# Kernel optimization log

Measured on AMD Instinct MI355X. Metric: run time of the kernel, lower is better.

## Reference

```python
import jax, jax.numpy as jnp
import numpy as np

HID = 64
INIT_N = 1000   # init_target_num
OUT_N = 50      # out_tar_num
XL = 64         # x_len
PI = float(np.pi)
SMALL = 1e-6
TEMP = 0.01


def _ln(x, g, b):
    m = jnp.mean(x, axis=-1, keepdims=True)
    v = jnp.mean((x - m) ** 2, axis=-1, keepdims=True)
    return (x - m) * jax.lax.rsqrt(v + 1e-5) * g + b


def _smooth_l1(p, t):
    d = jnp.abs(p - t)
    return jnp.mean(jnp.where(d < 1.0, 0.5 * d * d, d - 0.5))


def setup_inputs() -> dict:
    key = jax.random.key(0)
    ks = jax.random.split(key, 24)
    B, M = 512, 2000
    D = XL * 2 + 2  # 130
    f32 = jnp.float32

    def lin(k, i, o):
        return (jax.random.normal(k, (i, o), f32) / np.sqrt(i)).astype(f32)

    return {
        'osm': jax.random.normal(ks[0], (B, M, 4), f32),
        'agent_traj': jax.random.normal(ks[1], (B, XL), f32),
        'vectornet_feature': jax.random.normal(ks[2], (B, XL), f32),
        'end': jax.random.normal(ks[3], (B, 2), f32),
        'speed': jax.random.normal(ks[4], (B, 2), f32),
        # offsetx_pre: Linear(D,64) -> LN -> GELU -> Linear(64,2)
        'ox_w1': lin(ks[5], D, HID), 'ox_b1': jnp.zeros((HID,), f32),
        'ox_g1': jnp.ones((HID,), f32), 'ox_be1': jnp.zeros((HID,), f32),
        'ox_w2': lin(ks[6], HID, 2), 'ox_b2': jnp.zeros((2,), f32),
        # target_proj: Linear(D,64)->LN->GELU->Linear(64,64)->LN->GELU->Linear(64,2)
        'tp_w1': lin(ks[7], D, HID), 'tp_b1': jnp.zeros((HID,), f32),
        'tp_g1': jnp.ones((HID,), f32), 'tp_be1': jnp.zeros((HID,), f32),
        'tp_w2': lin(ks[8], HID, HID), 'tp_b2': jnp.zeros((HID,), f32),
        'tp_g2': jnp.ones((HID,), f32), 'tp_be2': jnp.zeros((HID,), f32),
        'tp_w3': lin(ks[9], HID, 2), 'tp_b3': jnp.zeros((2,), f32),
    }


def reference(osm, agent_traj, vectornet_feature, end, speed,
              ox_w1, ox_b1, ox_g1, ox_be1, ox_w2, ox_b2,
              tp_w1, tp_b1, tp_g1, tp_be1, tp_w2, tp_b2, tp_g2, tp_be2, tp_w3, tp_b3):
    B = osm.shape[0]
    # --- select INIT_N closest osm points (else-branch of original) ---
    osm_points = osm[:, :, :2]                                # [B,M,2]
    dist = jnp.sqrt(jnp.sum(osm_points ** 2, axis=2))         # [B,M]
    idx = jnp.argsort(dist, axis=1)[:, :INIT_N]               # [B,N]
    pts = jnp.take_along_axis(osm_points, idx[..., None], axis=1)  # [B,N,2]

    at = jnp.broadcast_to(agent_traj[:, None, :], (B, INIT_N, XL))
    vf = jnp.broadcast_to(vectornet_feature[:, None, :], (B, INIT_N, XL))

    # --- offsetx_pre MLP ---
    feat = jnp.concatenate([vf, at, pts], axis=-1)            # [B,N,130]
    h = jax.nn.gelu(_ln(feat @ ox_w1 + ox_b1, ox_g1, ox_be1), approximate=False)
    offset_x = h @ ox_w2 + ox_b2                              # [B,N,2]
    targets = pts + offset_x

    # --- target_proj MLP ---
    feat2 = jnp.concatenate([vf, at, targets], axis=-1)
    h = jax.nn.gelu(_ln(feat2 @ tp_w1 + tp_b1, tp_g1, tp_be1), approximate=False)
    h = jax.nn.gelu(_ln(h @ tp_w2 + tp_b2, tp_g2, tp_be2), approximate=False)
    targets = h @ tp_w3 + tp_b3                               # [B,N,2]

    # --- gaussian-like policy score over candidates ---
    mean = jnp.mean(targets, axis=1, keepdims=True)           # [B,1,2]
    var = jnp.var(targets, axis=1, keepdims=True, ddof=1)     # unbiased, like torch.var
    pdx = jnp.exp(-0.5 * (targets[..., 0] - mean[..., 0]) ** 2 / var[..., 0] + SMALL) \
          / jnp.sqrt(2.0 * PI * var[..., 0] + SMALL)
    pdy = jnp.exp(-0.5 * (targets[..., 1] - mean[..., 1]) ** 2 / var[..., 1] + SMALL) \
          / jnp.sqrt(2.0 * PI * var[..., 1] + SMALL)
    policy_dist = pdx * pdy                                   # [B,N]

    end_b = end[:, None, :]                                   # [B,1,2]
    L_off = _smooth_l1(targets, end_b)

    d = jnp.sqrt(jnp.sum((pts - end_b) ** 2, axis=2))         # [B,N]
    soft = jax.nn.softmax(-d / TEMP, axis=1)
    target_index = jnp.argmax(soft, axis=1)                   # [B]

    # CrossEntropyLoss(policy_dist as logits, target_index), mean reduction
    lse = jax.nn.logsumexp(policy_dist, axis=1)               # [B]
    picked = jnp.take_along_axis(policy_dist, target_index[:, None], axis=1)[:, 0]
    L_cls = jnp.mean(lse - picked)

    # top-k targets by policy_dist (descending)
    p_index = jnp.argsort(-policy_dist, axis=1)[:, :OUT_N]    # [B,K]
    top_targets = jnp.take_along_axis(targets, p_index[..., None], axis=1)  # [B,K,2]
    L_end = _smooth_l1(top_targets, end_b)

    return (L_cls, L_off + L_end * 3.0, top_targets)
```

## Files before the change

kernel.cpp:

```cpp
#include <hip/hip_runtime.h>
#include <math.h>

#define NT 256
#define NB 512
#define NP 2000
#define NS 1000
#define NO 50

typedef unsigned int u32;
typedef unsigned long long u64;
typedef unsigned short u16;
typedef unsigned char u8;
typedef __attribute__((ext_vector_type(8))) short short8;
typedef __attribute__((ext_vector_type(4))) float f32x4;

__device__ __forceinline__ float sl1(float x){ float d = fabsf(x); return d < 1.f ? 0.5f*d*d : d - 0.5f; }

__device__ __forceinline__ u32 mono(float f){
  u32 u = __float_as_uint(f);
  return u ^ ((u >> 31) ? 0xFFFFFFFFu : 0x80000000u);
}
__device__ __forceinline__ float dist_rn(float x, float y){
  return __fsqrt_rn(__fadd_rn(__fmul_rn(x,x), __fmul_rn(y,y)));
}
__device__ __forceinline__ float rl(float v, int l){
  return __builtin_bit_cast(float, __builtin_amdgcn_readlane(__builtin_bit_cast(int, v), l));
}
__device__ __forceinline__ u16 f2bf(float f){
  u32 u = __float_as_uint(f);
  u32 r = (u + 0x7FFFu + ((u >> 16) & 1u)) >> 16;
  return (u16)r;
}
__device__ __forceinline__ float bf2f(u16 h){ return __uint_as_float(((u32)h) << 16); }

__device__ __forceinline__ float gelu_(float x){
  float z = x * 0.70710678118654752440f;
  float az = fabsf(z);
  float t = __frcp_rn(fmaf(0.3275911f, az, 1.0f));
  float p =          fmaf(t, 1.061405429f, -1.453152027f);
  p = fmaf(p, t, 1.421413741f);
  p = fmaf(p, t, -0.284496736f);
  p = fmaf(p, t, 0.254829592f);
  p = p * t;
  float e = __expf(-az*az);
  float er = fmaf(-p, e, 1.0f);
  er = copysignf(er, z);
  float hx = 0.5f * x;
  return fmaf(hx, er, hx);
}
__device__ __forceinline__ float wred(float v){
  #pragma unroll
  for (int s = 1; s < 64; s <<= 1) v += __shfl_xor(v, s, 64);
  return v;
}
__device__ __forceinline__ float bsum(float v, float* s, int tid){
  #pragma unroll
  for (int o = 32; o > 0; o >>= 1) v += __shfl_down(v, o, 64);
  __syncthreads();
  if ((tid & 63) == 0) s[tid >> 6] = v;
  __syncthreads();
  return (s[0]+s[1])+(s[2]+s[3]);
}
__device__ __forceinline__ float bmax(float v, float* s, int tid){
  #pragma unroll
  for (int o = 32; o > 0; o >>= 1) v = fmaxf(v, __shfl_down(v, o, 64));
  __syncthreads();
  if ((tid & 63) == 0) s[tid >> 6] = v;
  __syncthreads();
  return fmaxf(fmaxf(s[0],s[1]), fmaxf(s[2],s[3]));
}
__device__ __forceinline__ u32 bminu32(u32 v, u32* s, int tid){
  #pragma unroll
  for (int o = 32; o > 0; o >>= 1){ u32 w = __shfl_down(v, o, 64); v = w < v ? w : v; }
  __syncthreads();
  if ((tid & 63) == 0) s[tid >> 6] = v;
  __syncthreads();
  u32 a = s[0] < s[1] ? s[0] : s[1];
  u32 c = s[2] < s[3] ? s[2] : s[3];
  return a < c ? a : c;
}
__device__ __forceinline__ u64 bminu64(u64 v, u64* s, int tid){
  #pragma unroll
  for (int o = 32; o > 0; o >>= 1){ u64 w = __shfl_down(v, o, 64); v = w < v ? w : v; }
  __syncthreads();
  if ((tid & 63) == 0) s[tid >> 6] = v;
  __syncthreads();
  u64 a = s[0] < s[1] ? s[0] : s[1];
  u64 c = s[2] < s[3] ? s[2] : s[3];
  return a < c ? a : c;
}

__global__ void init_k(double* acc){
  if (threadIdx.x < 8) acc[threadIdx.x] = 0.0;
}

__global__ __launch_bounds__(NT) void main_k(
    const float* __restrict__ osm, const float* __restrict__ agent, const float* __restrict__ vect,
    const float* __restrict__ endp,
    const float* __restrict__ oxw1, const float* __restrict__ oxb1, const float* __restrict__ oxg1, const float* __restrict__ oxbe1,
    const float* __restrict__ oxw2, const float* __restrict__ oxb2,
    const float* __restrict__ tpw1, const float* __restrict__ tpb1, const float* __restrict__ tpg1, const float* __restrict__ tpbe1,
    const float* __restrict__ tpw2, const float* __restrict__ tpb2, const float* __restrict__ tpg2, const float* __restrict__ tpbe2,
    const float* __restrict__ tpw3, const float* __restrict__ tpb3,
    float* __restrict__ out, double* __restrict__ acc)
{
  const int b = blockIdx.x;
  const int tid = threadIdx.x;
  const int lane = tid & 63;
  const int wv = tid >> 6;
  const int lm = lane & 15;
  const int q  = lane >> 4;

  __shared__ u32 keys32[2048];
  __shared__ u8  state[2048];
  __shared__ u32 hist[256];
  __shared__ u32 wtot[4];
  __shared__ u32 sc[8];
  __shared__ u16 sIdx[1024];
  __shared__ float2 ptf2[NS];
  __shared__ float2 tg[NS];
  __shared__ float pol[NS];
  __shared__ float vfs[64], ats[64];
  __shared__ float foxA[64], foxB[64], foxC[64];
  __shared__ float ftpA[64], ftpB[64], ftpC[64];
  __shared__ float w2aS[64], w2bS[64];
  __shared__ float scox[6], sctp[6];
  __shared__ float redf[4];
  __shared__ u32 redu[4];
  __shared__ u64 redk[4];
  __shared__ u16 list50[64];
  __shared__ __align__(16) u16 trans[4][2][16][72];

  const float2* osm2 = (const float2*)osm;
  const float ex = endp[b*2 + 0], ey = endp[b*2 + 1];

  if (tid < 64){ vfs[tid] = vect[b*64 + tid]; ats[tid] = agent[b*64 + tid]; }
  for (int i = tid; i < NP; i += NT){
    float2 P = osm2[((size_t)b*NP + i)*2];
    keys32[i] = mono(dist_rn(P.x, P.y));
  }
  for (int i = tid; i < 2048; i += NT) state[i] = (i < NP) ? (u8)2 : (u8)0;
  if (tid == 0){ sc[0] = NS; sc[2] = 0; }
  __syncthreads();

  {
    float* part = (float*)&trans[0][0][0][0];
    int ch = tid & 63, grp = tid >> 6;
    float pox = 0.f, ptp = 0.f;
    for (int k = grp*32; k < grp*32 + 32; ++k){
      float f = (k < 64) ? vfs[k] : ats[k-64];
      pox = fmaf(f, oxw1[k*64 + ch], pox);
      ptp = fmaf(f, tpw1[k*64 + ch], ptp);
    }
    part[grp*64 + ch] = pox;
    part[(grp+4)*64 + ch] = ptp;
    __syncthreads();
    if (tid < 64){
      float bo = oxb1[tid] + ((part[0*64+tid]+part[1*64+tid])+(part[2*64+tid]+part[3*64+tid]));
      float bt = tpb1[tid] + ((part[4*64+tid]+part[5*64+tid])+(part[6*64+tid]+part[7*64+tid]));
      float cxo = oxw1[128*64 + tid], cyo = oxw1[129*64 + tid];
      float cxt = tpw1[128*64 + tid], cyt = tpw1[129*64 + tid];
      const float inv64 = 1.0f/64.0f;
      float mb = wred(bo)*inv64, mx_ = wred(cxo)*inv64, my_ = wred(cyo)*inv64;
      float e0 = bo - mb, e1 = cxo - mx_, e2 = cyo - my_;
      float g = oxg1[tid];
      foxA[tid] = e0*g; foxB[tid] = e1*g; foxC[tid] = e2*g;
      float E00 = wred(e0*e0)*inv64, E11 = wred(e1*e1)*inv64, E22 = wred(e2*e2)*inv64;
      float E01 = wred(e0*e1)*inv64, E02 = wred(e0*e2)*inv64, E12 = wred(e1*e2)*inv64;
      if (tid == 0){ scox[0]=E00; scox[1]=E11; scox[2]=E22; scox[3]=E01; scox[4]=E02; scox[5]=E12; }
      float mb2 = wred(bt)*inv64, mx2 = wred(cxt)*inv64, my2 = wred(cyt)*inv64;
      float f0 = bt - mb2, f1 = cxt - mx2, f2 = cyt - my2;
      float gt_ = tpg1[tid];
      ftpA[tid] = f0*gt_; ftpB[tid] = f1*gt_; ftpC[tid] = f2*gt_;
      float F00 = wred(f0*f0)*inv64, F11 = wred(f1*f1)*inv64, F22 = wred(f2*f2)*inv64;
      float F01 = wred(f0*f1)*inv64, F02 = wred(f0*f2)*inv64, F12 = wred(f1*f2)*inv64;
      if (tid == 0){ sctp[0]=F00; sctp[1]=F11; sctp[2]=F22; sctp[3]=F01; sctp[4]=F02; sctp[5]=F12; }
      w2aS[tid] = oxw2[2*tid]; w2bS[tid] = oxw2[2*tid + 1];
    }
  }
  __syncthreads();

  {
    const int plist[6] = {7,6,5,4,1,0};
    for (int pi = 0; pi < 6; ++pi){
      if (sc[2]) break;
      const int p = plist[pi];
      hist[tid] = 0; __syncthreads();
      for (int i = tid; i < NP; i += NT) if (state[i] == 2){
        int bb = (p >= 4) ? (int)((keys32[i] >> ((p-4)*8)) & 255) : (int)((((u32)i) >> (p*8)) & 255);
        atomicAdd(&hist[bb], 1u);
      }
      __syncthreads();
      u32 myc = hist[tid], v = myc;
      { int l_ = tid & 63;
        #pragma unroll
        for (int s = 1; s < 64; s <<= 1){ u32 n = __shfl_up(v, s, 64); if (l_ >= s) v += n; }
        if (l_ == 63) wtot[tid >> 6] = v;
      }
      __syncthreads();
      u32 add = 0;
      #pragma unroll
      for (int w = 0; w < 4; ++w) if (w < (tid >> 6)) add += wtot[w];
      u32 myinc = v + add;
      u32 Krem = sc[0];
      bool iamp = false; u32 exc = myinc - myc;
      if (myc > 0 && exc <= Krem-1 && Krem-1 < myinc){ sc[1] = (u32)tid; iamp = true; }
      __syncthreads();
      u32 pb = sc[1];
      for (int i = tid; i < NP; i += NT) if (state[i] == 2){
        int bb = (p >= 4) ? (int)((keys32[i] >> ((p-4)*8)) & 255) : (int)((((u32)i) >> (p*8)) & 255);
        state[i] = (bb < (int)pb) ? (u8)1 : (bb > (int)pb) ? (u8)0 : (u8)2;
      }
      if (iamp){ u32 nk = Krem - exc; sc[0] = nk; if (nk == myc) sc[2] = 1; }
      __syncthreads();
    }
    if (tid == 0) sc[4] = 0;
    __syncthreads();
    for (int i = tid; i < NP; i += NT) if (state[i] != 0){
      u32 pos = atomicAdd(&sc[4], 1u);
      sIdx[pos] = (u16)i;
      ptf2[pos] = osm2[((size_t)b*NP + i)*2];
    }
    __syncthreads();
  }

  const float foxAv = foxA[lane], foxBv = foxB[lane], foxCv = foxC[lane], beoxv = oxbe1[lane];
  const float ftpAv = ftpA[lane], ftpBv = ftpB[lane], ftpCv = ftpC[lane], be2v = tpbe1[lane];
  const float so0 = scox[0], so1 = scox[1], so2 = scox[2], so3 = scox[3], so4 = scox[4], so5 = scox[5];
  const float st0 = sctp[0], st1 = sctp[1], st2 = sctp[2], st3 = sctp[3], st4 = sctp[4], st5 = sctp[5];
  const float oxb20 = oxb2[0], oxb21 = oxb2[1], tpb30 = tpb3[0], tpb31 = tpb3[1];
  float g3c[4], be3c[4], b2i[4], w3a[4], w3b[4];
  #pragma unroll
  for (int nt = 0; nt < 4; ++nt){
    int ch = lm + 16*nt;
    g3c[nt] = tpg2[ch]; be3c[nt] = tpbe2[ch]; b2i[nt] = tpb2[ch];
    w3a[nt] = tpw3[ch*2]; w3b[nt] = tpw3[ch*2 + 1];
  }
  short8 bh[2][4], bl[2][4];
  #pragma unroll
  for (int kt = 0; kt < 2; ++kt)
    #pragma unroll
    for (int nt = 0; nt < 4; ++nt){
      short8 H, L;
      #pragma unroll
      for (int j = 0; j < 8; ++j){
        float w = tpw2[(kt*32 + q*8 + j)*64 + nt*16 + lm];
        u16 hh = f2bf(w);
        H[j] = (short)hh;
        L[j] = (short)f2bf(w - bf2f(hh));
      }
      bh[kt][nt] = H; bl[kt][nt] = L;
    }

  u16* trh  = &trans[wv][0][0][0];
  u16* trl_ = &trans[wv][1][0][0];
  float* trf = (float*)&trans[wv][0][0][0];
  float loff = 0.f;

  for (int t = wv; t < 63; t += 4){
    const int pbase = t*16;
    int sp = pbase + lm; if (sp > NS-1) sp = NS-1;
    const float2 P = ptf2[sp];
    const float px = P.x, py = P.y;
    float var1 = so0 + px*px*so1 + py*py*so2 + 2.0f*(px*so3 + py*so4 + px*py*so5);
    const float r1 = __frsqrt_rn(var1 + 1e-5f);
    #pragma unroll
    for (int p = 0; p < 16; ++p){
      float spx = rl(px,p), spy = rl(py,p), sr = rl(r1,p);
      float vv = fmaf(sr, fmaf(spy, foxCv, fmaf(spx, foxBv, foxAv)), beoxv);
      trf[p*68 + lane] = gelu_(vv);
    }
    f32x4 ga = *(f32x4*)&trf[lm*68 + q*16 + 0];
    f32x4 gb = *(f32x4*)&trf[lm*68 + q*16 + 4];
    f32x4 gc = *(f32x4*)&trf[lm*68 + q*16 + 8];
    f32x4 gd = *(f32x4*)&trf[lm*68 + q*16 + 12];
    f32x4 wa0 = *(f32x4*)&w2aS[q*16+0], wa1 = *(f32x4*)&w2aS[q*16+4], wa2 = *(f32x4*)&w2aS[q*16+8], wa3 = *(f32x4*)&w2aS[q*16+12];
    f32x4 wb0 = *(f32x4*)&w2bS[q*16+0], wb1 = *(f32x4*)&w2bS[q*16+4], wb2 = *(f32x4*)&w2bS[q*16+8], wb3 = *(f32x4*)&w2bS[q*16+12];
    float o0 = 0.f, o1 = 0.f;
    #pragma unroll
    for (int j = 0; j < 4; ++j){
      o0 = fmaf(ga[j],wa0[j], fmaf(gb[j],wa1[j], fmaf(gc[j],wa2[j], fmaf(gd[j],wa3[j], o0))));
      o1 = fmaf(ga[j],wb0[j], fmaf(gb[j],wb1[j], fmaf(gc[j],wb2[j], fmaf(gd[j],wb3[j], o1))));
    }
    o0 += __shfl_xor(o0,16,64); o0 += __shfl_xor(o0,32,64);
    o1 += __shfl_xor(o1,16,64); o1 += __shfl_xor(o1,32,64);
    const float tx = px + o0 + oxb20;
    const float ty = py + o1 + oxb21;
    float var2 = st0 + tx*tx*st1 + ty*ty*st2 + 2.0f*(tx*st3 + ty*st4 + tx*ty*st5);
    const float r2 = __frsqrt_rn(var2 + 1e-5f);
    #pragma unroll
    for (int p = 0; p < 16; ++p){
      float stx = rl(tx,p), sty = rl(ty,p), sr = rl(r2,p);
      float vv = fmaf(sr, fmaf(sty, ftpCv, fmaf(stx, ftpBv, ftpAv)), be2v);
      vv = gelu_(vv);
      u16 hh = f2bf(vv);
      trh[p*72 + lane]  = hh;
      trl_[p*72 + lane] = f2bf(vv - bf2f(hh));
    }
    short8 ah0 = *(short8*)&trh[lm*72 + q*8];
    short8 ah1 = *(short8*)&trh[lm*72 + 32 + q*8];
    short8 al0 = *(short8*)&trl_[lm*72 + q*8];
    short8 al1 = *(short8*)&trl_[lm*72 + 32 + q*8];
    f32x4 accv[4];
    #pragma unroll
    for (int nt = 0; nt < 4; ++nt){
      f32x4 c; c[0] = c[1] = c[2] = c[3] = b2i[nt];
      c = __builtin_amdgcn_mfma_f32_16x16x32_bf16(ah0, bh[0][nt], c, 0,0,0);
      c = __builtin_amdgcn_mfma_f32_16x16x32_bf16(ah1, bh[1][nt], c, 0,0,0);
      c = __builtin_amdgcn_mfma_f32_16x16x32_bf16(ah0, bl[0][nt], c, 0,0,0);
      c = __builtin_amdgcn_mfma_f32_16x16x32_bf16(ah1, bl[1][nt], c, 0,0,0);
      c = __builtin_amdgcn_mfma_f32_16x16x32_bf16(al0, bh[0][nt], c, 0,0,0);
      c = __builtin_amdgcn_mfma_f32_16x16x32_bf16(al1, bh[1][nt], c, 0,0,0);
      accv[nt] = c;
    }
    float sP[4], qP[4];
    #pragma unroll
    for (int e = 0; e < 4; ++e){
      float a0 = accv[0][e], a1 = accv[1][e], a2 = accv[2][e], a3 = accv[3][e];
      sP[e] = (a0+a1)+(a2+a3);
      qP[e] = fmaf(a0,a0, fmaf(a1,a1, fmaf(a2,a2, a3*a3)));
    }
    #pragma unroll
    for (int s_ = 1; s_ < 16; s_ <<= 1){
      #pragma unroll
      for (int e = 0; e < 4; ++e){ sP[e] += __shfl_xor(sP[e], s_, 64); qP[e] += __shfl_xor(qP[e], s_, 64); }
    }
    float mE[4], rE[4];
    #pragma unroll
    for (int e = 0; e < 4; ++e){
      float m = sP[e] * (1.0f/64.0f);
      float vv = fmaf(sP[e], -m*(1.0f/64.0f), qP[e]*(1.0f/64.0f));
      mE[e] = m; rE[e] = __frsqrt_rn(vv + 1e-5f);
    }
    float uo[4] = {0,0,0,0}, vo[4] = {0,0,0,0};
    #pragma unroll
    for (int nt = 0; nt < 4; ++nt)
      #pragma unroll
      for (int e = 0; e < 4; ++e){
        float g = gelu_(fmaf((accv[nt][e]-mE[e])*rE[e], g3c[nt], be3c[nt]));
        uo[e] = fmaf(g, w3a[nt], uo[e]);
        vo[e] = fmaf(g, w3b[nt], vo[e]);
      }
    #pragma unroll
    for (int s_ = 1; s_ < 16; s_ <<= 1){
      #pragma unroll
      for (int e = 0; e < 4; ++e){ uo[e] += __shfl_xor(uo[e], s_, 64); vo[e] += __shfl_xor(vo[e], s_, 64); }
    }
    if (lm == 0){
      #pragma unroll
      for (int e = 0; e < 4; ++e){
        int pt = pbase + q*4 + e;
        if (pt < NS){
          float t0 = uo[e] + tpb30, t1 = vo[e] + tpb31;
          tg[pt] = make_float2(t0, t1);
          loff += sl1(t0-ex) + sl1(t1-ey);
        }
      }
    }
  }
  __syncthreads();

  const float loffT = bsum(loff, redf, tid);
  float sx = 0.f, sy = 0.f;
  for (int s = tid; s < NS; s += NT){ float2 T = tg[s]; sx += T.x; sy += T.y; }
  const float mx = bsum(sx, redf, tid) * (1.0f/NS);
  const float my = bsum(sy, redf, tid) * (1.0f/NS);
  float qx = 0.f, qy = 0.f;
  for (int s = tid; s < NS; s += NT){ float2 T = tg[s]; float dx = T.x-mx, dy = T.y-my; qx = fmaf(dx,dx,qx); qy = fmaf(dy,dy,qy); }
  const float vx = bsum(qx, redf, tid) * (1.0f/(NS-1));
  const float vy = bsum(qy, redf, tid) * (1.0f/(NS-1));
  const float TWO_PI = 6.2831853071795864769f;
  const float rdx = __frcp_rn(__fsqrt_rn(TWO_PI*vx + 1e-6f));
  const float rdy = __frcp_rn(__fsqrt_rn(TWO_PI*vy + 1e-6f));
  float pmaxl = -1e30f;
  for (int s = tid; s < NS; s += NT){
    float2 T = tg[s]; float dx = T.x-mx, dy = T.y-my;
    float pdx = expf(-0.5f*dx*dx/vx + 1e-6f) * rdx;
    float pdy = expf(-0.5f*dy*dy/vy + 1e-6f) * rdy;
    float pp = pdx*pdy;
    pol[s] = pp;
    pmaxl = fmaxf(pmaxl, pp);
  }
  const float pmax = bmax(pmaxl, redf, tid);
  float se = 0.f;
  for (int s = tid; s < NS; s += NT) se += expf(pol[s] - pmax);
  const float sume = bsum(se, redf, tid);

  u32 xkm = 0xFFFFFFFFu;
  for (int s = tid; s < NS; s += NT){
    float2 Pp = ptf2[s];
    float dd = dist_rn(Pp.x-ex, Pp.y-ey);
    u32 xk = ~mono((0.0f - dd) / 0.01f);
    if (xk < xkm) xkm = xk;
  }
  xkm = bminu32(xkm, redu, tid);
  u64 dmin = 0xFFFFFFFFFFFFFFFFull;
  for (int s = tid; s < NS; s += NT){
    float2 Pp = ptf2[s];
    float dd = dist_rn(Pp.x-ex, Pp.y-ey);
    u32 xk = ~mono((0.0f - dd) / 0.01f);
    if (xk == xkm){ u32 oi = sIdx[s]; u64 dk = (((u64)keys32[oi]) << 32) | (u64)oi; if (dk < dmin) dmin = dk; }
  }
  dmin = bminu64(dmin, redk, tid);
  for (int s = tid; s < NS; s += NT){
    float2 Pp = ptf2[s];
    float dd = dist_rn(Pp.x-ex, Pp.y-ey);
    u32 xk = ~mono((0.0f - dd) / 0.01f);
    u32 oi = sIdx[s];
    if (xk == xkm && ((((u64)keys32[oi]) << 32) | (u64)oi) == dmin) sc[5] = (u32)s;
  }
  __syncthreads();
  if (tid == 0){
    float lse = pmax + logf(sume);
    float picked = pol[sc[5]];
    atomicAdd(&acc[0], (double)(lse - picked));
    atomicAdd(&acc[1], (double)loffT);
  }

  for (int i = tid; i < 2048; i += NT) state[i] = (i < NS) ? (u8)2 : (u8)0;
  if (tid == 0){ sc[0] = NO; sc[2] = 0; }
  __syncthreads();
  {
    const int plist2[10] = {11,10,9,8,7,6,5,4,1,0};
    for (int pi = 0; pi < 10; ++pi){
      if (sc[2]) break;
      const int p = plist2[pi];
      hist[tid] = 0; __syncthreads();
      for (int i = tid; i < NS; i += NT) if (state[i] == 2){
        u32 oi = sIdx[i];
        int bb = (p >= 8) ? (int)(((~mono(pol[i])) >> ((p-8)*8)) & 255)
               : (p >= 4) ? (int)((keys32[oi] >> ((p-4)*8)) & 255)
               : (int)((((u32)oi) >> (p*8)) & 255);
        atomicAdd(&hist[bb], 1u);
      }
      __syncthreads();
      u32 myc = hist[tid], v = myc;
      { int l_ = tid & 63;
        #pragma unroll
        for (int s = 1; s < 64; s <<= 1){ u32 n = __shfl_up(v, s, 64); if (l_ >= s) v += n; }
        if (l_ == 63) wtot[tid >> 6] = v;
      }
      __syncthreads();
      u32 add = 0;
      #pragma unroll
      for (int w = 0; w < 4; ++w) if (w < (tid >> 6)) add += wtot[w];
      u32 myinc = v + add;
      u32 Krem = sc[0];
      bool iamp = false; u32 exc = myinc - myc;
      if (myc > 0 && exc <= Krem-1 && Krem-1 < myinc){ sc[1] = (u32)tid; iamp = true; }
      __syncthreads();
      u32 pb = sc[1];
      for (int i = tid; i < NS; i += NT) if (state[i] == 2){
        u32 oi = sIdx[i];
        int bb = (p >= 8) ? (int)(((~mono(pol[i])) >> ((p-8)*8)) & 255)
               : (p >= 4) ? (int)((keys32[oi] >> ((p-4)*8)) & 255)
               : (int)((((u32)oi) >> (p*8)) & 255);
        state[i] = (bb < (int)pb) ? (u8)1 : (bb > (int)pb) ? (u8)0 : (u8)2;
      }
      if (iamp){ u32 nk = Krem - exc; sc[0] = nk; if (nk == myc) sc[2] = 1; }
      __syncthreads();
    }
  }
  if (tid == 0) sc[4] = 0;
  __syncthreads();
  for (int i = tid; i < NS; i += NT) if (state[i] != 0){
    u32 pos = atomicAdd(&sc[4], 1u);
    list50[pos] = (u16)i;
  }
  __syncthreads();

  if (wv == 0){
    u64 hi; u32 lo; int s;
    if (lane < NO){
      s = (int)list50[lane];
      u32 oi = sIdx[s];
      hi = (((u64)(~mono(pol[s]))) << 32) | (u64)keys32[oi];
      lo = oi;
    } else { hi = 0xFFFFFFFFFFFFFFFFull; lo = 0xFFFFFFFFu; s = 0; }
    #pragma unroll
    for (int k = 2; k <= 64; k <<= 1){
      #pragma unroll
      for (int j = k >> 1; j > 0; j >>= 1){
        u64 ohi = __shfl_xor(hi, j, 64);
        u32 olo = __shfl_xor(lo, j, 64);
        int os  = __shfl_xor(s,  j, 64);
        bool up = ((lane & k) == 0);
        bool lower = ((lane & j) == 0);
        bool gt = (hi > ohi) || ((hi == ohi) && (lo > olo));
        bool lt = (hi < ohi) || ((hi == ohi) && (lo < olo));
        bool take = (up == lower) ? gt : lt;
        if (take){ hi = ohi; lo = olo; s = os; }
      }
    }
    float le = 0.f;
    if (lane < NO){
      float2 T = tg[s];
      out[2 + ((size_t)b*NO + lane)*2 + 0] = T.x;
      out[2 + ((size_t)b*NO + lane)*2 + 1] = T.y;
      le = sl1(T.x-ex) + sl1(T.y-ey);
    }
    #pragma unroll
    for (int o = 32; o > 0; o >>= 1) le += __shfl_down(le, o, 64);
    if (lane == 0) atomicAdd(&acc[2], (double)le);
  }
}

__global__ void fin_k(const double* acc, float* out){
  if (threadIdx.x == 0){
    out[0] = (float)(acc[0] / (double)NB);
    out[1] = (float)(acc[1] / ((double)NB*NS*2) + 3.0 * (acc[2] / ((double)NB*NO*2)));
  }
}

extern "C" void kernel_launch(void* const* d_in, const int* in_sizes, int n_in,
                              void* d_out, int out_size, void* d_ws, size_t ws_size,
                              hipStream_t stream){
  const float* osm   = (const float*)d_in[0];
  const float* agent = (const float*)d_in[1];
  const float* vect  = (const float*)d_in[2];
  const float* endp  = (const float*)d_in[3];
  const float* oxw1  = (const float*)d_in[5];
  const float* oxb1  = (const float*)d_in[6];
  const float* oxg1  = (const float*)d_in[7];
  const float* oxbe1 = (const float*)d_in[8];
  const float* oxw2  = (const float*)d_in[9];
  const float* oxb2  = (const float*)d_in[10];
  const float* tpw1  = (const float*)d_in[11];
  const float* tpb1  = (const float*)d_in[12];
  const float* tpg1  = (const float*)d_in[13];
  const float* tpbe1 = (const float*)d_in[14];
  const float* tpw2  = (const float*)d_in[15];
  const float* tpb2  = (const float*)d_in[16];
  const float* tpg2  = (const float*)d_in[17];
  const float* tpbe2 = (const float*)d_in[18];
  const float* tpw3  = (const float*)d_in[19];
  const float* tpb3  = (const float*)d_in[20];
  float* out = (float*)d_out;
  double* acc = (double*)d_ws;

  hipLaunchKernelGGL(init_k, dim3(1), dim3(64), 0, stream, acc);
  hipLaunchKernelGGL(main_k, dim3(NB), dim3(NT), 0, stream,
    osm, agent, vect, endp,
    oxw1, oxb1, oxg1, oxbe1, oxw2, oxb2,
    tpw1, tpb1, tpg1, tpbe1, tpw2, tpb2, tpg2, tpbe2, tpw3, tpb3,
    out, acc);
  hipLaunchKernelGGL(fin_k, dim3(1), dim3(64), 0, stream, acc, out);
}
```

Measured before the change: 255.8 us.

## Double block threads, compute GELU tables per lane, fuse finalize into main kernel

Raises the block size from 256 to 512 threads (8 waves), with the reductions and the tile loop over 63 point groups adjusted to match. The per-point GELU evaluation now reads packed float4 tables directly in each lane instead of broadcasting with readlane and transposing through shared memory. The finalize kernel is replaced by a last-block-done counter with atomics, and the init kernel by a memset. The rest of the work is unchanged, but more threads per block may cut occupancy and leave threads idle in the 256-bin radix histogram steps.

```diff
diff --git a/kernel.cpp b/kernel.cpp
--- a/kernel.cpp
+++ b/kernel.cpp
@@ -1,7 +1,8 @@
 #include <hip/hip_runtime.h>
 #include <math.h>
 
-#define NT 256
+#define NT 512
+#define NW 8
 #define NB 512
 #define NP 2000
 #define NS 1000
@@ -22,9 +23,6 @@
 }
 __device__ __forceinline__ float dist_rn(float x, float y){
   return __fsqrt_rn(__fadd_rn(__fmul_rn(x,x), __fmul_rn(y,y)));
-}
-__device__ __forceinline__ float rl(float v, int l){
-  return __builtin_bit_cast(float, __builtin_amdgcn_readlane(__builtin_bit_cast(int, v), l));
 }
 __device__ __forceinline__ u16 f2bf(float f){
   u32 u = __float_as_uint(f);
@@ -59,7 +57,7 @@
   __syncthreads();
   if ((tid & 63) == 0) s[tid >> 6] = v;
   __syncthreads();
-  return (s[0]+s[1])+(s[2]+s[3]);
+  return ((s[0]+s[1])+(s[2]+s[3])) + ((s[4]+s[5])+(s[6]+s[7]));
 }
 __device__ __forceinline__ float bmax(float v, float* s, int tid){
   #pragma unroll
@@ -67,7 +65,9 @@
   __syncthreads();
   if ((tid & 63) == 0) s[tid >> 6] = v;
   __syncthreads();
-  return fmaxf(fmaxf(s[0],s[1]), fmaxf(s[2],s[3]));
+  float a = fmaxf(fmaxf(s[0],s[1]), fmaxf(s[2],s[3]));
+  float b = fmaxf(fmaxf(s[4],s[5]), fmaxf(s[6],s[7]));
+  return fmaxf(a, b);
 }
 __device__ __forceinline__ u32 bminu32(u32 v, u32* s, int tid){
   #pragma unroll
@@ -75,9 +75,10 @@
   __syncthreads();
   if ((tid & 63) == 0) s[tid >> 6] = v;
   __syncthreads();
-  u32 a = s[0] < s[1] ? s[0] : s[1];
-  u32 c = s[2] < s[3] ? s[2] : s[3];
-  return a < c ? a : c;
+  u32 m = s[0];
+  #pragma unroll
+  for (int w = 1; w < NW; ++w) m = s[w] < m ? s[w] : m;
+  return m;
 }
 __device__ __forceinline__ u64 bminu64(u64 v, u64* s, int tid){
   #pragma unroll
@@ -85,16 +86,13 @@
   __syncthreads();
   if ((tid & 63) == 0) s[tid >> 6] = v;
   __syncthreads();
-  u64 a = s[0] < s[1] ? s[0] : s[1];
-  u64 c = s[2] < s[3] ? s[2] : s[3];
-  return a < c ? a : c;
-}
-
-__global__ void init_k(double* acc){
-  if (threadIdx.x < 8) acc[threadIdx.x] = 0.0;
-}
-
-__global__ __launch_bounds__(NT) void main_k(
+  u64 m = s[0];
+  #pragma unroll
+  for (int w = 1; w < NW; ++w) m = s[w] < m ? s[w] : m;
+  return m;
+}
+
+__global__ __launch_bounds__(NT, 4) void main_k(
     const float* __restrict__ osm, const float* __restrict__ agent, const float* __restrict__ vect,
     const float* __restrict__ endp,
     const float* __restrict__ oxw1, const float* __restrict__ oxb1, const float* __restrict__ oxg1, const float* __restrict__ oxbe1,
@@ -102,7 +100,7 @@
     const float* __restrict__ tpw1, const float* __restrict__ tpb1, const float* __restrict__ tpg1, const float* __restrict__ tpbe1,
     const float* __restrict__ tpw2, const float* __restrict__ tpb2, const float* __restrict__ tpg2, const float* __restrict__ tpbe2,
     const float* __restrict__ tpw3, const float* __restrict__ tpb3,
-    float* __restrict__ out, double* __restrict__ acc)
+    float* __restrict__ out, double* __restrict__ acc, u32* __restrict__ cnt)
 {
   const int b = blockIdx.x;
   const int tid = threadIdx.x;
@@ -114,22 +112,21 @@
   __shared__ u32 keys32[2048];
   __shared__ u8  state[2048];
   __shared__ u32 hist[256];
-  __shared__ u32 wtot[4];
+  __shared__ u32 wtot[NW];
   __shared__ u32 sc[8];
   __shared__ u16 sIdx[1024];
   __shared__ float2 ptf2[NS];
   __shared__ float2 tg[NS];
   __shared__ float pol[NS];
   __shared__ float vfs[64], ats[64];
-  __shared__ float foxA[64], foxB[64], foxC[64];
-  __shared__ float ftpA[64], ftpB[64], ftpC[64];
-  __shared__ float w2aS[64], w2bS[64];
+  __shared__ float4 tabO[64];
+  __shared__ float2 tabW[64];
+  __shared__ float4 tabT[64];
   __shared__ float scox[6], sctp[6];
-  __shared__ float redf[4];
-  __shared__ u32 redu[4];
-  __shared__ u64 redk[4];
+  __shared__ float redf[NW];
+  __shared__ u32 redu[NW];
+  __shared__ u64 redk[NW];
   __shared__ u16 list50[64];
-  __shared__ __align__(16) u16 trans[4][2][16][72];
 
   const float2* osm2 = (const float2*)osm;
   const float ex = endp[b*2 + 0], ey = endp[b*2 + 1];
@@ -144,38 +141,39 @@
   __syncthreads();
 
   {
-    float* part = (float*)&trans[0][0][0][0];
-    int ch = tid & 63, grp = tid >> 6;
+    float* part = (float*)tg;
+    const int ch = tid & 63, grp = tid >> 6;
     float pox = 0.f, ptp = 0.f;
-    for (int k = grp*32; k < grp*32 + 32; ++k){
+    for (int k = grp*16; k < grp*16 + 16; ++k){
       float f = (k < 64) ? vfs[k] : ats[k-64];
       pox = fmaf(f, oxw1[k*64 + ch], pox);
       ptp = fmaf(f, tpw1[k*64 + ch], ptp);
     }
     part[grp*64 + ch] = pox;
-    part[(grp+4)*64 + ch] = ptp;
+    part[(grp+8)*64 + ch] = ptp;
     __syncthreads();
     if (tid < 64){
-      float bo = oxb1[tid] + ((part[0*64+tid]+part[1*64+tid])+(part[2*64+tid]+part[3*64+tid]));
-      float bt = tpb1[tid] + ((part[4*64+tid]+part[5*64+tid])+(part[6*64+tid]+part[7*64+tid]));
+      float bo = oxb1[tid], bt = tpb1[tid];
+      #pragma unroll
+      for (int g = 0; g < 8; ++g){ bo += part[g*64 + tid]; bt += part[(g+8)*64 + tid]; }
       float cxo = oxw1[128*64 + tid], cyo = oxw1[129*64 + tid];
       float cxt = tpw1[128*64 + tid], cyt = tpw1[129*64 + tid];
       const float inv64 = 1.0f/64.0f;
       float mb = wred(bo)*inv64, mx_ = wred(cxo)*inv64, my_ = wred(cyo)*inv64;
       float e0 = bo - mb, e1 = cxo - mx_, e2 = cyo - my_;
       float g = oxg1[tid];
-      foxA[tid] = e0*g; foxB[tid] = e1*g; foxC[tid] = e2*g;
+      tabO[tid] = make_float4(e0*g, e1*g, e2*g, oxbe1[tid]);
+      tabW[tid] = make_float2(oxw2[2*tid], oxw2[2*tid + 1]);
       float E00 = wred(e0*e0)*inv64, E11 = wred(e1*e1)*inv64, E22 = wred(e2*e2)*inv64;
       float E01 = wred(e0*e1)*inv64, E02 = wred(e0*e2)*inv64, E12 = wred(e1*e2)*inv64;
       if (tid == 0){ scox[0]=E00; scox[1]=E11; scox[2]=E22; scox[3]=E01; scox[4]=E02; scox[5]=E12; }
       float mb2 = wred(bt)*inv64, mx2 = wred(cxt)*inv64, my2 = wred(cyt)*inv64;
       float f0 = bt - mb2, f1 = cxt - mx2, f2 = cyt - my2;
       float gt_ = tpg1[tid];
-      ftpA[tid] = f0*gt_; ftpB[tid] = f1*gt_; ftpC[tid] = f2*gt_;
+      tabT[tid] = make_float4(f0*gt_, f1*gt_, f2*gt_, tpbe1[tid]);
       float F00 = wred(f0*f0)*inv64, F11 = wred(f1*f1)*inv64, F22 = wred(f2*f2)*inv64;
       float F01 = wred(f0*f1)*inv64, F02 = wred(f0*f2)*inv64, F12 = wred(f1*f2)*inv64;
       if (tid == 0){ sctp[0]=F00; sctp[1]=F11; sctp[2]=F22; sctp[3]=F01; sctp[4]=F02; sctp[5]=F12; }
-      w2aS[tid] = oxw2[2*tid]; w2bS[tid] = oxw2[2*tid + 1];
     }
   }
   __syncthreads();
@@ -185,33 +183,39 @@
     for (int pi = 0; pi < 6; ++pi){
       if (sc[2]) break;
       const int p = plist[pi];
-      hist[tid] = 0; __syncthreads();
+      if (tid < 256) hist[tid] = 0;
+      __syncthreads();
       for (int i = tid; i < NP; i += NT) if (state[i] == 2){
         int bb = (p >= 4) ? (int)((keys32[i] >> ((p-4)*8)) & 255) : (int)((((u32)i) >> (p*8)) & 255);
         atomicAdd(&hist[bb], 1u);
       }
       __syncthreads();
-      u32 myc = hist[tid], v = myc;
-      { int l_ = tid & 63;
+      u32 myc = 0, v = 0;
+      if (tid < 256){
+        myc = hist[tid]; v = myc;
+        int l_ = tid & 63;
         #pragma unroll
         for (int s = 1; s < 64; s <<= 1){ u32 n = __shfl_up(v, s, 64); if (l_ >= s) v += n; }
         if (l_ == 63) wtot[tid >> 6] = v;
       }
       __syncthreads();
-      u32 add = 0;
-      #pragma unroll
-      for (int w = 0; w < 4; ++w) if (w < (tid >> 6)) add += wtot[w];
-      u32 myinc = v + add;
-      u32 Krem = sc[0];
-      bool iamp = false; u32 exc = myinc - myc;
-      if (myc > 0 && exc <= Krem-1 && Krem-1 < myinc){ sc[1] = (u32)tid; iamp = true; }
+      bool iamp = false; u32 nk = 0;
+      if (tid < 256){
+        u32 add = 0;
+        #pragma unroll
+        for (int w = 0; w < 4; ++w) if (w < (tid >> 6)) add += wtot[w];
+        u32 myinc = v + add;
+        u32 Krem = sc[0];
+        u32 exc = myinc - myc;
+        if (myc > 0 && exc <= Krem-1 && Krem-1 < myinc){ sc[1] = (u32)tid; iamp = true; nk = Krem - exc; }
+      }
       __syncthreads();
       u32 pb = sc[1];
       for (int i = tid; i < NP; i += NT) if (state[i] == 2){
         int bb = (p >= 4) ? (int)((keys32[i] >> ((p-4)*8)) & 255) : (int)((((u32)i) >> (p*8)) & 255);
         state[i] = (bb < (int)pb) ? (u8)1 : (bb > (int)pb) ? (u8)0 : (u8)2;
       }
-      if (iamp){ u32 nk = Krem - exc; sc[0] = nk; if (nk == myc) sc[2] = 1; }
+      if (iamp){ sc[0] = nk; if (nk == myc) sc[2] = 1; }
       __syncthreads();
     }
     if (tid == 0) sc[4] = 0;
@@ -224,8 +228,6 @@
     __syncthreads();
   }
 
-  const float foxAv = foxA[lane], foxBv = foxB[lane], foxCv = foxC[lane], beoxv = oxbe1[lane];
-  const float ftpAv = ftpA[lane], ftpBv = ftpB[lane], ftpCv = ftpC[lane], be2v = tpbe1[lane];
   const float so0 = scox[0], so1 = scox[1], so2 = scox[2], so3 = scox[3], so4 = scox[4], so5 = scox[5];
   const float st0 = sctp[0], st1 = sctp[1], st2 = sctp[2], st3 = sctp[3], st4 = sctp[4], st5 = sctp[5];
   const float oxb20 = oxb2[0], oxb21 = oxb2[1], tpb30 = tpb3[0], tpb31 = tpb3[1];
@@ -252,35 +254,23 @@
       bh[kt][nt] = H; bl[kt][nt] = L;
     }
 
-  u16* trh  = &trans[wv][0][0][0];
-  u16* trl_ = &trans[wv][1][0][0];
-  float* trf = (float*)&trans[wv][0][0][0];
   float loff = 0.f;
-
-  for (int t = wv; t < 63; t += 4){
+  for (int t = wv; t < 63; t += NW){
     const int pbase = t*16;
     int sp = pbase + lm; if (sp > NS-1) sp = NS-1;
     const float2 P = ptf2[sp];
     const float px = P.x, py = P.y;
     float var1 = so0 + px*px*so1 + py*py*so2 + 2.0f*(px*so3 + py*so4 + px*py*so5);
     const float r1 = __frsqrt_rn(var1 + 1e-5f);
-    #pragma unroll
-    for (int p = 0; p < 16; ++p){
-      float spx = rl(px,p), spy = rl(py,p), sr = rl(r1,p);
-      float vv = fmaf(sr, fmaf(spy, foxCv, fmaf(spx, foxBv, foxAv)), beoxv);
-      trf[p*68 + lane] = gelu_(vv);
-    }
-    f32x4 ga = *(f32x4*)&trf[lm*68 + q*16 + 0];
-    f32x4 gb = *(f32x4*)&trf[lm*68 + q*16 + 4];
-    f32x4 gc = *(f32x4*)&trf[lm*68 + q*16 + 8];
-    f32x4 gd = *(f32x4*)&trf[lm*68 + q*16 + 12];
-    f32x4 wa0 = *(f32x4*)&w2aS[q*16+0], wa1 = *(f32x4*)&w2aS[q*16+4], wa2 = *(f32x4*)&w2aS[q*16+8], wa3 = *(f32x4*)&w2aS[q*16+12];
-    f32x4 wb0 = *(f32x4*)&w2bS[q*16+0], wb1 = *(f32x4*)&w2bS[q*16+4], wb2 = *(f32x4*)&w2bS[q*16+8], wb3 = *(f32x4*)&w2bS[q*16+12];
     float o0 = 0.f, o1 = 0.f;
     #pragma unroll
-    for (int j = 0; j < 4; ++j){
-      o0 = fmaf(ga[j],wa0[j], fmaf(gb[j],wa1[j], fmaf(gc[j],wa2[j], fmaf(gd[j],wa3[j], o0))));
-      o1 = fmaf(ga[j],wb0[j], fmaf(gb[j],wb1[j], fmaf(gc[j],wb2[j], fmaf(gd[j],wb3[j], o1))));
+    for (int j = 0; j < 16; ++j){
+      const int c = q*16 + j;
+      const float4 T = tabO[c];
+      const float2 W = tabW[c];
+      float g1 = gelu_(fmaf(r1, fmaf(py, T.z, fmaf(px, T.y, T.x)), T.w));
+      o0 = fmaf(g1, W.x, o0);
+      o1 = fmaf(g1, W.y, o1);
     }
     o0 += __shfl_xor(o0,16,64); o0 += __shfl_xor(o0,32,64);
     o1 += __shfl_xor(o1,16,64); o1 += __shfl_xor(o1,32,64);
@@ -288,19 +278,17 @@
     const float ty = py + o1 + oxb21;
     float var2 = st0 + tx*tx*st1 + ty*ty*st2 + 2.0f*(tx*st3 + ty*st4 + tx*ty*st5);
     const float r2 = __frsqrt_rn(var2 + 1e-5f);
-    #pragma unroll
-    for (int p = 0; p < 16; ++p){
-      float stx = rl(tx,p), sty = rl(ty,p), sr = rl(r2,p);
-      float vv = fmaf(sr, fmaf(sty, ftpCv, fmaf(stx, ftpBv, ftpAv)), be2v);
-      vv = gelu_(vv);
-      u16 hh = f2bf(vv);
-      trh[p*72 + lane]  = hh;
-      trl_[p*72 + lane] = f2bf(vv - bf2f(hh));
-    }
-    short8 ah0 = *(short8*)&trh[lm*72 + q*8];
-    short8 ah1 = *(short8*)&trh[lm*72 + 32 + q*8];
-    short8 al0 = *(short8*)&trl_[lm*72 + q*8];
-    short8 al1 = *(short8*)&trl_[lm*72 + 32 + q*8];
+    short8 ah0, ah1, al0, al1;
+    #pragma unroll
+    for (int j = 0; j < 8; ++j){
+      const int c0 = q*8 + j, c1 = 32 + q*8 + j;
+      const float4 T0 = tabT[c0], T1 = tabT[c1];
+      float v0 = gelu_(fmaf(r2, fmaf(ty, T0.z, fmaf(tx, T0.y, T0.x)), T0.w));
+      float v1 = gelu_(fmaf(r2, fmaf(ty, T1.z, fmaf(tx, T1.y, T1.x)), T1.w));
+      u16 h0 = f2bf(v0), h1 = f2bf(v1);
+      ah0[j] = (short)h0; al0[j] = (short)f2bf(v0 - bf2f(h0));
+      ah1[j] = (short)h1; al1[j] = (short)f2bf(v1 - bf2f(h1));
+    }
     f32x4 accv[4];
     #pragma unroll
     for (int nt = 0; nt < 4; ++nt){
@@ -425,7 +413,8 @@
     for (int pi = 0; pi < 10; ++pi){
       if (sc[2]) break;
       const int p = plist2[pi];
-      hist[tid] = 0; __syncthreads();
+      if (tid < 256) hist[tid] = 0;
+      __syncthreads();
       for (int i = tid; i < NS; i += NT) if (state[i] == 2){
         u32 oi = sIdx[i];
         int bb = (p >= 8) ? (int)(((~mono(pol[i])) >> ((p-8)*8)) & 255)
@@ -434,20 +423,25 @@
         atomicAdd(&hist[bb], 1u);
       }
       __syncthreads();
-      u32 myc = hist[tid], v = myc;
-      { int l_ = tid & 63;
+      u32 myc = 0, v = 0;
+      if (tid < 256){
+        myc = hist[tid]; v = myc;
+        int l_ = tid & 63;
         #pragma unroll
         for (int s = 1; s < 64; s <<= 1){ u32 n = __shfl_up(v, s, 64); if (l_ >= s) v += n; }
         if (l_ == 63) wtot[tid >> 6] = v;
       }
       __syncthreads();
-      u32 add = 0;
-      #pragma unroll
-      for (int w = 0; w < 4; ++w) if (w < (tid >> 6)) add += wtot[w];
-      u32 myinc = v + add;
-      u32 Krem = sc[0];
-      bool iamp = false; u32 exc = myinc - myc;
-      if (myc > 0 && exc <= Krem-1 && Krem-1 < myinc){ sc[1] = (u32)tid; iamp = true; }
+      bool iamp = false; u32 nk = 0;
+      if (tid < 256){
+        u32 add = 0;
+        #pragma unroll
+        for (int w = 0; w < 4; ++w) if (w < (tid >> 6)) add += wtot[w];
+        u32 myinc = v + add;
+        u32 Krem = sc[0];
+        u32 exc = myinc - myc;
+        if (myc > 0 && exc <= Krem-1 && Krem-1 < myinc){ sc[1] = (u32)tid; iamp = true; nk = Krem - exc; }
+      }
       __syncthreads();
       u32 pb = sc[1];
       for (int i = tid; i < NS; i += NT) if (state[i] == 2){
@@ -457,7 +451,7 @@
                : (int)((((u32)oi) >> (p*8)) & 255);
         state[i] = (bb < (int)pb) ? (u8)1 : (bb > (int)pb) ? (u8)0 : (u8)2;
       }
-      if (iamp){ u32 nk = Krem - exc; sc[0] = nk; if (nk == myc) sc[2] = 1; }
+      if (iamp){ sc[0] = nk; if (nk == myc) sc[2] = 1; }
       __syncthreads();
     }
   }
@@ -501,14 +495,18 @@
     }
     #pragma unroll
     for (int o = 32; o > 0; o >>= 1) le += __shfl_down(le, o, 64);
-    if (lane == 0) atomicAdd(&acc[2], (double)le);
-  }
-}
-
-__global__ void fin_k(const double* acc, float* out){
-  if (threadIdx.x == 0){
-    out[0] = (float)(acc[0] / (double)NB);
-    out[1] = (float)(acc[1] / ((double)NB*NS*2) + 3.0 * (acc[2] / ((double)NB*NO*2)));
+    if (lane == 0){
+      atomicAdd(&acc[2], (double)le);
+      __threadfence();
+      u32 old = atomicAdd(cnt, 1u);
+      if (old == NB - 1){
+        double c0 = atomicAdd(&acc[0], 0.0);
+        double c1 = atomicAdd(&acc[1], 0.0);
+        double c2 = atomicAdd(&acc[2], 0.0);
+        out[0] = (float)(c0 / (double)NB);
+        out[1] = (float)(c1 / ((double)NB*NS*2) + 3.0 * (c2 / ((double)NB*NO*2)));
+      }
+    }
   }
 }
 
@@ -537,12 +535,12 @@
   const float* tpb3  = (const float*)d_in[20];
   float* out = (float*)d_out;
   double* acc = (double*)d_ws;
-
-  hipLaunchKernelGGL(init_k, dim3(1), dim3(64), 0, stream, acc);
+  u32* cnt = (u32*)((char*)d_ws + 24);
+
+  hipMemsetAsync(d_ws, 0, 32, stream);
   hipLaunchKernelGGL(main_k, dim3(NB), dim3(NT), 0, stream,
     osm, agent, vect, endp,
     oxw1, oxb1, oxg1, oxbe1, oxw2, oxb2,
     tpw1, tpb1, tpg1, tpbe1, tpw2, tpb2, tpg2, tpbe2, tpw3, tpb3,
-    out, acc);
-  hipLaunchKernelGGL(fin_k, dim3(1), dim3(64), 0, stream, acc, out);
-}
+    out, acc, cnt);
+}
```

New measurement: 490.9 us. 91.9% more time.
